# Kernel optimization log

Hardware: AMD Instinct MI355X
Metric: run time of the kernel (lower is better)

The kernel has to match this reference:

```python
import jax, jax.numpy as jnp
import numpy as np

K_HEADS = 8
D_HEAD = 16
D_MODEL = K_HEADS * D_HEAD  # 128


def _xavier(key, shape):
    fan_in, fan_out = shape[0], shape[1]
    limit = (6.0 / (fan_in + fan_out)) ** 0.5
    return jax.random.uniform(key, shape, jnp.float32, -limit, limit)


def setup_inputs() -> dict:
    key = jax.random.key(0)
    ks = jax.random.split(key, 8)
    B, T, N = 8, 12, 512
    X = jax.random.normal(ks[0], (B, T, N, D_MODEL), jnp.float32)
    STE = jax.random.normal(ks[1], (B, T, N, 2 * D_MODEL), jnp.float32)
    Wq = _xavier(ks[2], (3 * D_MODEL, D_MODEL))
    Wk = _xavier(ks[3], (3 * D_MODEL, D_MODEL))
    Wv = _xavier(ks[4], (3 * D_MODEL, D_MODEL))
    Wo = _xavier(ks[5], (D_MODEL, D_MODEL))
    bq = jnp.zeros((D_MODEL,), jnp.float32)
    bk = jnp.zeros((D_MODEL,), jnp.float32)
    bv = jnp.zeros((D_MODEL,), jnp.float32)
    bo = jnp.zeros((D_MODEL,), jnp.float32)
    return {"X": X, "STE": STE, "Wq": Wq, "bq": bq, "Wk": Wk, "bk": bk,
            "Wv": Wv, "bv": bv, "Wo": Wo, "bo": bo}


def reference(X, STE, Wq, bq, Wk, bk, Wv, bv, Wo, bo):
    # 1x1-conv FCs == per-(t,node) linear + relu on the last dim
    H = jnp.concatenate([X, STE], axis=-1)              # [B,T,N,3D]
    q = jax.nn.relu(H @ Wq + bq)                        # [B,T,N,D]
    k = jax.nn.relu(H @ Wk + bk)
    v = jax.nn.relu(H @ Wv + bv)
    B, T, N, D = q.shape

    def heads(x):  # split last dim into K heads (head index major), move to front
        return x.reshape(B, T, N, K_HEADS, D_HEAD).transpose(3, 0, 1, 2, 4)

    qh, kh, vh = heads(q), heads(k), heads(v)           # [K,B,T,N,d]
    att = jnp.einsum('kbtnd,kbtmd->kbtnm', qh, kh) / (D_HEAD ** 0.5)
    att = jax.nn.softmax(att, axis=-1)                  # [K,B,T,N,N]
    o = jnp.einsum('kbtnm,kbtmd->kbtnd', att, vh)       # [K,B,T,N,d]
    o = o.transpose(1, 2, 3, 0, 4).reshape(B, T, N, D)  # concat heads on last dim
    return jax.nn.relu(o @ Wo + bo)
```

## Files before the change

### kernel.cpp

```cpp
#include <hip/hip_runtime.h>
#include <math.h>

constexpr int B_  = 8;
constexpr int T_  = 12;
constexpr int N_  = 512;
constexpr int DM  = 128;
constexpr int KH  = 8;
constexpr int DH  = 16;
constexpr int MR  = B_*T_*N_;
constexpr int K3  = 3*DM;
constexpr int TB  = 256;

typedef __attribute__((ext_vector_type(8))) short  bf16x8;
typedef __attribute__((ext_vector_type(4))) float  f32x4;
typedef __attribute__((ext_vector_type(4))) int    i32x4;

static __device__ inline unsigned short f2bf(float x) {
    unsigned u = __float_as_uint(x);
    return (unsigned short)((u + 0x7fffu + ((u >> 16) & 1u)) >> 16);
}
static __device__ inline unsigned pk2(float a, float b) {
    unsigned ua = __float_as_uint(a) + 0x8000u;
    unsigned ub = __float_as_uint(b) + 0x8000u;
    return __builtin_amdgcn_perm(ub, ua, 0x07060302u);
}

__global__ __launch_bounds__(256) void wprep_kernel(
    const float* __restrict__ Wq, const float* __restrict__ Wk,
    const float* __restrict__ Wv, const float* __restrict__ Wo,
    unsigned short* __restrict__ Wt, unsigned short* __restrict__ Wot)
{
    const int idx = blockIdx.x*256 + threadIdx.x;
    if (idx < 3*K3*DM) {
        const int p   = idx / (K3*DM);
        const int rem = idx - p*(K3*DM);
        const int k   = rem >> 7;
        const int n   = rem & 127;
        const float* W = (p == 0) ? Wq : ((p == 1) ? Wk : Wv);
        Wt[p*(K3*DM) + n*K3 + k] = f2bf(W[rem]);
    } else {
        const int i2 = idx - 3*K3*DM;
        const int k  = i2 >> 7;
        const int n  = i2 & 127;
        Wot[n*DM + k] = f2bf(Wo[i2]);
    }
}

__global__ __launch_bounds__(256, 2) void qkv_mfma(
    const float* __restrict__ X, const float* __restrict__ STE,
    const unsigned short* __restrict__ Wt,
    const float* __restrict__ bq, const float* __restrict__ bk,
    const float* __restrict__ bv,
    unsigned short* __restrict__ qb, unsigned short* __restrict__ kb2,
    unsigned short* __restrict__ vb2)
{
    __shared__ __align__(16) unsigned short Ash[128*72];
    __shared__ __align__(16) unsigned short Bsh[128*72];
    const int tid = threadIdx.x;
    const int rb  = blockIdx.x * 128;
    const int p   = blockIdx.y;
    const unsigned short* __restrict__ wtp = Wt + p*(K3*DM);
    const float* __restrict__ bias = (p == 0) ? bq : ((p == 1) ? bk : bv);
    unsigned short* __restrict__ outb = (p == 0) ? qb : ((p == 1) ? kb2 : vb2);
    const float scale = (p == 0) ? 0.25f : 1.0f;

    const int lane = tid & 63, wv = tid >> 6;
    const int wm = (wv >> 1)*64, wn = (wv & 1)*64;
    const int m15 = lane & 15, g = lane >> 4;

    f32x4 acc[4][4] = {};

    for (int kt = 0; kt < K3; kt += 64) {
        const float* __restrict__ src = (kt < DM) ? (X + kt) : (STE + (kt - DM));
        const int ldr = (kt < DM) ? DM : 2*DM;
        #pragma unroll
        for (int i = 0; i < 8; ++i) {
            const int idx = tid + i*TB;
            const int m   = idx >> 4;
            const int c4  = idx & 15;
            const float4 f = *(const float4*)(src + (rb + m)*ldr + c4*4);
            uint2 d2;
            d2.x = pk2(f.x, f.y);
            d2.y = pk2(f.z, f.w);
            *(uint2*)(Ash + m*72 + c4*4) = d2;
        }
        #pragma unroll
        for (int i = 0; i < 4; ++i) {
            const int idx = tid + i*TB;
            const int n   = idx >> 3;
            const int kg  = idx & 7;
            *(uint4*)(Bsh + n*72 + kg*8) =
                *(const uint4*)(wtp + n*K3 + kt + kg*8);
        }
        __syncthreads();
        #pragma unroll
        for (int ks = 0; ks < 64; ks += 32) {
            bf16x8 af[4], bf[4];
            #pragma unroll
            for (int i = 0; i < 4; ++i)
                af[i] = *(const bf16x8*)(Ash + (wm + i*16 + m15)*72 + ks + g*8);
            #pragma unroll
            for (int j = 0; j < 4; ++j)
                bf[j] = *(const bf16x8*)(Bsh + (wn + j*16 + m15)*72 + ks + g*8);
            #pragma unroll
            for (int i = 0; i < 4; ++i)
                #pragma unroll
                for (int j = 0; j < 4; ++j)
                    acc[i][j] = __builtin_amdgcn_mfma_f32_16x16x32_bf16(
                        af[i], bf[j], acc[i][j], 0, 0, 0);
        }
        __syncthreads();
    }

    #pragma unroll
    for (int j = 0; j < 4; ++j) {
        const int c  = wn + j*16 + m15;
        const float bj = bias[c];
        const int h = c >> 4, d = c & 15;
        #pragma unroll
        for (int i = 0; i < 4; ++i) {
            #pragma unroll
            for (int r = 0; r < 4; ++r) {
                const int row = rb + wm + i*16 + g*4 + r;
                float v = acc[i][j][r] + bj;
                v = (v > 0.f ? v : 0.f) * scale;
                outb[(h*MR + row)*DH + d] = f2bf(v);
            }
        }
    }
}

__global__ __launch_bounds__(256, 3) void attn_kernel(
    const unsigned short* __restrict__ qb, const unsigned short* __restrict__ kb,
    const unsigned short* __restrict__ vb, unsigned short* __restrict__ ob)
{
    __shared__ __align__(16) unsigned short Klds[N_*DH];
    __shared__ __align__(16) unsigned short Vtlds[DH*536];

    const int tid = threadIdx.x;
    const int h   = blockIdx.x & (KH-1);
    const int bt  = blockIdx.x >> 3;
    const int base = (h*MR + bt*N_) * DH;

    {
        const uint4* kg = (const uint4*)(kb + base);
        uint4* kl = (uint4*)Klds;
        #pragma unroll
        for (int i = 0; i < 4; ++i) kl[tid + i*TB] = kg[tid + i*TB];
    }
    {
        const unsigned* vg = (const unsigned*)(vb + base);
        unsigned a[8], b[8];
        #pragma unroll
        for (int j = 0; j < 8; ++j) {
            a[j] = vg[(2*tid)*8 + j];
            b[j] = vg[(2*tid+1)*8 + j];
        }
        unsigned* vt = (unsigned*)Vtlds;
        #pragma unroll
        for (int d = 0; d < 16; ++d) {
            const int sh = (d & 1) * 16;
            const unsigned lo = (a[d >> 1] >> sh) & 0xffffu;
            const unsigned hi = (b[d >> 1] >> sh) & 0xffffu;
            vt[d*268 + tid] = lo | (hi << 16);
        }
    }
    __syncthreads();

    const int wv   = tid >> 6;
    const int lane = tid & 63;
    const int m    = lane & 15;
    const int g    = lane >> 4;

    bf16x8 qf[8];
    const unsigned short* qp = qb + base;
    #pragma unroll
    for (int j = 0; j < 8; ++j) {
        bf16x8 t = {0,0,0,0,0,0,0,0};
        if (g < 2) t = *(const bf16x8*)(qp + ((wv*8 + j)*16 + m)*DH + g*8);
        qf[j] = t;
    }

    f32x4 acc[8] = {};
    float lpart[8] = {0.f,0.f,0.f,0.f,0.f,0.f,0.f,0.f};

    for (int c = 0; c < 16; ++c) {
        const int kr0 = c*32 + ((m & 12) << 1) + (m & 3);
        bf16x8 kf0 = {0,0,0,0,0,0,0,0};
        bf16x8 kf1 = {0,0,0,0,0,0,0,0};
        if (g < 2) {
            kf0 = *(const bf16x8*)(Klds + kr0*DH + g*8);
            kf1 = *(const bf16x8*)(Klds + (kr0 + 4)*DH + g*8);
        }
        const bf16x8 vf = *(const bf16x8*)(Vtlds + m*536 + c*32 + g*8);

        #pragma unroll
        for (int j = 0; j < 8; ++j) {
            f32x4 z = {0.f, 0.f, 0.f, 0.f};
            f32x4 s0 = __builtin_amdgcn_mfma_f32_16x16x32_bf16(kf0, qf[j], z, 0, 0, 0);
            f32x4 s1 = __builtin_amdgcn_mfma_f32_16x16x32_bf16(kf1, qf[j], z, 0, 0, 0);
            float p0 = __expf(s0[0] - 20.f);
            float p1 = __expf(s0[1] - 20.f);
            float p2 = __expf(s0[2] - 20.f);
            float p3 = __expf(s0[3] - 20.f);
            float p4 = __expf(s1[0] - 20.f);
            float p5 = __expf(s1[1] - 20.f);
            float p6 = __expf(s1[2] - 20.f);
            float p7 = __expf(s1[3] - 20.f);
            lpart[j] += ((p0 + p1) + (p2 + p3)) + ((p4 + p5) + (p6 + p7));
            i32x4 pd = { (int)pk2(p0, p1), (int)pk2(p2, p3),
                         (int)pk2(p4, p5), (int)pk2(p6, p7) };
            const bf16x8 pf = __builtin_bit_cast(bf16x8, pd);
            acc[j] = __builtin_amdgcn_mfma_f32_16x16x32_bf16(pf, vf, acc[j], 0, 0, 0);
        }
    }

    #pragma unroll
    for (int j = 0; j < 8; ++j) {
        float lf = lpart[j];
        lf += __shfl_xor(lf, 16);
        lf += __shfl_xor(lf, 32);
        const float invl = 1.0f / lf;
        const int ib = __float_as_int(invl);
        #pragma unroll
        for (int r = 0; r < 4; ++r) {
            const float iv = __int_as_float(
                __builtin_amdgcn_ds_bpermute((4*g + r) * 4, ib));
            const int qrow = bt*N_ + (wv*8 + j)*16 + 4*g + r;
            ob[qrow*DM + h*DH + m] = f2bf(acc[j][r] * iv);
        }
    }
}

__global__ __launch_bounds__(256, 2) void out_mfma(
    const unsigned short* __restrict__ ot, const unsigned short* __restrict__ Wot,
    const float* __restrict__ bo, float* __restrict__ out)
{
    __shared__ __align__(16) unsigned short Ash[128*136];
    __shared__ __align__(16) unsigned short Bsh[128*136];
    const int tid = threadIdx.x;
    const int rb  = blockIdx.x * 128;
    const int lane = tid & 63, wv = tid >> 6;
    const int wm = (wv >> 1)*64, wn = (wv & 1)*64;
    const int m15 = lane & 15, g = lane >> 4;

    #pragma unroll
    for (int i = 0; i < 8; ++i) {
        const int idx = tid + i*TB;
        const int r  = idx >> 4;
        const int kg = idx & 15;
        *(uint4*)(Ash + r*136 + kg*8) = *(const uint4*)(ot + (rb + r)*DM + kg*8);
        *(uint4*)(Bsh + r*136 + kg*8) = *(const uint4*)(Wot + r*DM + kg*8);
    }
    __syncthreads();

    f32x4 acc[4][4] = {};
    #pragma unroll
    for (int ks = 0; ks < 128; ks += 32) {
        bf16x8 af[4], bf[4];
        #pragma unroll
        for (int i = 0; i < 4; ++i)
            af[i] = *(const bf16x8*)(Ash + (wm + i*16 + m15)*136 + ks + g*8);
        #pragma unroll
        for (int j = 0; j < 4; ++j)
            bf[j] = *(const bf16x8*)(Bsh + (wn + j*16 + m15)*136 + ks + g*8);
        #pragma unroll
        for (int i = 0; i < 4; ++i)
            #pragma unroll
            for (int j = 0; j < 4; ++j)
                acc[i][j] = __builtin_amdgcn_mfma_f32_16x16x32_bf16(
                    af[i], bf[j], acc[i][j], 0, 0, 0);
    }

    #pragma unroll
    for (int j = 0; j < 4; ++j) {
        const int c  = wn + j*16 + m15;
        const float bj = bo[c];
        #pragma unroll
        for (int i = 0; i < 4; ++i) {
            #pragma unroll
            for (int r = 0; r < 4; ++r) {
                const int row = rb + wm + i*16 + g*4 + r;
                float v = acc[i][j][r] + bj;
                out[row*DM + c] = v > 0.f ? v : 0.f;
            }
        }
    }
}

extern "C" void kernel_launch(void* const* d_in, const int* in_sizes, int n_in,
                              void* d_out, int out_size, void* d_ws, size_t ws_size,
                              hipStream_t stream)
{
    const float* X   = (const float*)d_in[0];
    const float* STE = (const float*)d_in[1];
    const float* Wq  = (const float*)d_in[2];
    const float* bq  = (const float*)d_in[3];
    const float* Wk  = (const float*)d_in[4];
    const float* bk  = (const float*)d_in[5];
    const float* Wv  = (const float*)d_in[6];
    const float* bv  = (const float*)d_in[7];
    const float* Wo  = (const float*)d_in[8];
    const float* bo  = (const float*)d_in[9];
    float* out = (float*)d_out;

    unsigned short* qb  = (unsigned short*)d_ws;
    unsigned short* kb  = qb  + (size_t)MR*DM;
    unsigned short* vb  = kb  + (size_t)MR*DM;
    unsigned short* ot  = vb  + (size_t)MR*DM;
    unsigned short* Wt  = ot  + (size_t)MR*DM;
    unsigned short* Wot = Wt  + (size_t)3*K3*DM;

    hipLaunchKernelGGL(wprep_kernel, dim3((3*K3*DM + DM*DM)/TB), dim3(TB), 0, stream,
                       Wq, Wk, Wv, Wo, Wt, Wot);
    hipLaunchKernelGGL(qkv_mfma, dim3(MR/128, 3), dim3(TB), 0, stream,
                       X, STE, Wt, bq, bk, bv, qb, kb, vb);
    hipLaunchKernelGGL(attn_kernel, dim3(KH*B_*T_), dim3(TB), 0, stream,
                       qb, kb, vb, ot);
    hipLaunchKernelGGL(out_mfma, dim3(MR/128), dim3(TB), 0, stream,
                       ot, Wot, bo, out);
}
```

Measured before the change: 207.2 us.

## Fold softmax scale into exp2, use MFMA for row sums, truncate bf16 packing

Folds log2(e) into the Q projection scale and the constant shift into the MFMA accumulator init, so the softmax uses exp2 directly with no subtract. Row sums are computed by an extra MFMA against a ones vector instead of VALU adds plus cross-lane shuffles and bpermute. P is packed to bf16 by truncation rather than rounding, and the final normalisation uses a hardware reciprocal. This trades VALU work for extra matrix-core work and more accumulator registers. The sum now matches the bf16-rounded P that feeds the PV product, while truncation adds a slight bias.

Measured after the change: 212.8 us. +2.7%, slower.

```diff
diff --git a/kernel.cpp b/kernel.cpp
--- a/kernel.cpp
+++ b/kernel.cpp
@@ -15,6 +15,9 @@
 typedef __attribute__((ext_vector_type(4))) float  f32x4;
 typedef __attribute__((ext_vector_type(4))) int    i32x4;
 
+#define LOG2E 1.44269504088896340736f
+#define SHIFT2 28.8539008177792681f
+
 static __device__ inline unsigned short f2bf(float x) {
     unsigned u = __float_as_uint(x);
     return (unsigned short)((u + 0x7fffu + ((u >> 16) & 1u)) >> 16);
@@ -23,6 +26,17 @@
     unsigned ua = __float_as_uint(a) + 0x8000u;
     unsigned ub = __float_as_uint(b) + 0x8000u;
     return __builtin_amdgcn_perm(ub, ua, 0x07060302u);
+}
+static __device__ inline unsigned pk2t(float a, float b) {
+    return __builtin_amdgcn_perm(__float_as_uint(b), __float_as_uint(a),
+                                 0x07060302u);
+}
+static __device__ inline float fast_rcp(float x) {
+#if __has_builtin(__builtin_amdgcn_rcpf)
+    return __builtin_amdgcn_rcpf(x);
+#else
+    return 1.0f / x;
+#endif
 }
 
 __global__ __launch_bounds__(256) void wprep_kernel(
@@ -62,7 +76,7 @@
     const unsigned short* __restrict__ wtp = Wt + p*(K3*DM);
     const float* __restrict__ bias = (p == 0) ? bq : ((p == 1) ? bk : bv);
     unsigned short* __restrict__ outb = (p == 0) ? qb : ((p == 1) ? kb2 : vb2);
-    const float scale = (p == 0) ? 0.25f : 1.0f;
+    const float scale = (p == 0) ? (0.25f * LOG2E) : 1.0f;
 
     const int lane = tid & 63, wv = tid >> 6;
     const int wm = (wv >> 1)*64, wn = (wv & 1)*64;
@@ -181,8 +195,11 @@
         qf[j] = t;
     }
 
-    f32x4 acc[8] = {};
-    float lpart[8] = {0.f,0.f,0.f,0.f,0.f,0.f,0.f,0.f};
+    const bf16x8 ones = {0x3F80,0x3F80,0x3F80,0x3F80,0x3F80,0x3F80,0x3F80,0x3F80};
+    const f32x4 zshift = {-SHIFT2, -SHIFT2, -SHIFT2, -SHIFT2};
+
+    f32x4 acc[8]  = {};
+    f32x4 lacc[8] = {};
 
     for (int c = 0; c < 16; ++c) {
         const int kr0 = c*32 + ((m & 12) << 1) + (m & 3);
@@ -196,36 +213,29 @@
 
         #pragma unroll
         for (int j = 0; j < 8; ++j) {
-            f32x4 z = {0.f, 0.f, 0.f, 0.f};
-            f32x4 s0 = __builtin_amdgcn_mfma_f32_16x16x32_bf16(kf0, qf[j], z, 0, 0, 0);
-            f32x4 s1 = __builtin_amdgcn_mfma_f32_16x16x32_bf16(kf1, qf[j], z, 0, 0, 0);
-            float p0 = __expf(s0[0] - 20.f);
-            float p1 = __expf(s0[1] - 20.f);
-            float p2 = __expf(s0[2] - 20.f);
-            float p3 = __expf(s0[3] - 20.f);
-            float p4 = __expf(s1[0] - 20.f);
-            float p5 = __expf(s1[1] - 20.f);
-            float p6 = __expf(s1[2] - 20.f);
-            float p7 = __expf(s1[3] - 20.f);
-            lpart[j] += ((p0 + p1) + (p2 + p3)) + ((p4 + p5) + (p6 + p7));
-            i32x4 pd = { (int)pk2(p0, p1), (int)pk2(p2, p3),
-                         (int)pk2(p4, p5), (int)pk2(p6, p7) };
+            f32x4 s0 = __builtin_amdgcn_mfma_f32_16x16x32_bf16(kf0, qf[j], zshift, 0, 0, 0);
+            f32x4 s1 = __builtin_amdgcn_mfma_f32_16x16x32_bf16(kf1, qf[j], zshift, 0, 0, 0);
+            const float p0 = exp2f(s0[0]);
+            const float p1 = exp2f(s0[1]);
+            const float p2 = exp2f(s0[2]);
+            const float p3 = exp2f(s0[3]);
+            const float p4 = exp2f(s1[0]);
+            const float p5 = exp2f(s1[1]);
+            const float p6 = exp2f(s1[2]);
+            const float p7 = exp2f(s1[3]);
+            i32x4 pd = { (int)pk2t(p0, p1), (int)pk2t(p2, p3),
+                         (int)pk2t(p4, p5), (int)pk2t(p6, p7) };
             const bf16x8 pf = __builtin_bit_cast(bf16x8, pd);
-            acc[j] = __builtin_amdgcn_mfma_f32_16x16x32_bf16(pf, vf, acc[j], 0, 0, 0);
+            acc[j]  = __builtin_amdgcn_mfma_f32_16x16x32_bf16(pf, vf,   acc[j],  0, 0, 0);
+            lacc[j] = __builtin_amdgcn_mfma_f32_16x16x32_bf16(pf, ones, lacc[j], 0, 0, 0);
         }
     }
 
     #pragma unroll
     for (int j = 0; j < 8; ++j) {
-        float lf = lpart[j];
-        lf += __shfl_xor(lf, 16);
-        lf += __shfl_xor(lf, 32);
-        const float invl = 1.0f / lf;
-        const int ib = __float_as_int(invl);
         #pragma unroll
         for (int r = 0; r < 4; ++r) {
-            const float iv = __int_as_float(
-                __builtin_amdgcn_ds_bpermute((4*g + r) * 4, ib));
+            const float iv = fast_rcp(lacc[j][r]);
             const int qrow = bt*N_ + (wv*8 + j)*16 + 4*g + r;
             ob[qrow*DM + h*DH + m] = f2bf(acc[j][r] * iv);
         }
```
